# Optimization experiments

Hardware: AMD Instinct MI355X
Metric: run time of the kernel (lower is better)

## Reference

```python
import jax, jax.numpy as jnp
import numpy as np

IN_FEATURE = 256
OUT_FEATURE = 128
ALPHA = 0.5  # LeakyReLU negative slope
NEG_BIG = -9e15


def setup_inputs() -> dict:
    key = jax.random.key(0)
    k1, k2, k3, k4 = jax.random.split(key, 4)
    N = 8192
    x = jax.random.normal(k1, (N, IN_FEATURE), dtype=jnp.float32)
    adj = jax.random.randint(k2, (N, N), 0, 2, dtype=jnp.int32)
    stdv = 1.0 / np.sqrt(OUT_FEATURE)
    W = jax.random.uniform(k3, (IN_FEATURE, OUT_FEATURE), dtype=jnp.float32,
                           minval=-stdv, maxval=stdv)
    a = jax.random.uniform(k4, (2 * OUT_FEATURE, 1), dtype=jnp.float32,
                           minval=-stdv, maxval=stdv)
    return {"input": x, "adj": adj, "W": W, "a": a}


def reference(input, adj, W, a):
    # h: [N, F_out]
    h = input @ W
    # Additive attention: cat([h_i, h_j]) @ a == h_i @ a1 + h_j @ a2
    a1 = a[:OUT_FEATURE, 0]   # [F_out]
    a2 = a[OUT_FEATURE:, 0]   # [F_out]
    f1 = h @ a1               # [N]  (row / source contribution)
    f2 = h @ a2               # [N]  (col / target contribution)
    e = jax.nn.leaky_relu(f1[:, None] + f2[None, :], negative_slope=ALPHA)  # [N, N]
    scores = jnp.where(adj > 0, e, NEG_BIG)
    attention = jax.nn.softmax(scores, axis=1)  # [N, N]
    h_prime = attention @ h                     # [N, F_out]
    return jax.nn.elu(h_prime)
```

## Files before the change

### kernel.cpp

```cpp
#include <hip/hip_runtime.h>

#define N_NODES 8192
#define IN_F 256
#define OUT_F 128
#define ALPHA 0.5f
#define JC 8
#define KCHUNK 1024
#define ROUNDS 32

using short8 = __attribute__((ext_vector_type(8))) short;
using f32x4  = __attribute__((ext_vector_type(4))) float;

__device__ __forceinline__ unsigned int f2bf(float f){
  unsigned int u = __float_as_uint(f);
  u += 0x7fffu + ((u >> 16) & 1u);
  return u >> 16;
}

__global__ __launch_bounds__(256) void k_hfp(const float* __restrict__ x,
                                             const float* __restrict__ W,
                                             const float* __restrict__ a,
                                             float* __restrict__ f1,
                                             float* __restrict__ f2,
                                             unsigned short* __restrict__ P){
  __shared__ float xs[32*IN_F];
  __shared__ unsigned short hl[32*136];
  const int tid = threadIdx.x;
  const int r0 = blockIdx.x * 32;
  const float4* xg = (const float4*)(x + (size_t)r0*IN_F);
  #pragma unroll
  for(int i=0;i<8;i++) ((float4*)xs)[tid + i*256] = xg[tid + i*256];
  __syncthreads();
  const int wave = tid >> 6, lane = tid & 63;
  float2 acc[8];
  #pragma unroll
  for(int j=0;j<8;j++){ acc[j].x = 0.f; acc[j].y = 0.f; }
  const float2* Wp = (const float2*)W;
  for(int k4=0;k4<IN_F;k4+=4){
    float4 xq[8];
    #pragma unroll
    for(int j=0;j<8;j++) xq[j] = *(const float4*)&xs[(wave*8+j)*IN_F + k4];
    #pragma unroll
    for(int kk=0;kk<4;kk++){
      float2 wv = Wp[(size_t)(k4+kk)*64 + lane];
      #pragma unroll
      for(int j=0;j<8;j++){
        float xv = kk==0?xq[j].x : kk==1?xq[j].y : kk==2?xq[j].z : xq[j].w;
        acc[j].x += xv*wv.x; acc[j].y += xv*wv.y;
      }
    }
  }
  {
    float2 a1 = ((const float2*)a)[lane];
    float2 a2 = ((const float2*)(a + OUT_F))[lane];
    float s1[8], s2[8];
    #pragma unroll
    for(int j=0;j<8;j++){
      s1[j] = acc[j].x*a1.x + acc[j].y*a1.y;
      s2[j] = acc[j].x*a2.x + acc[j].y*a2.y;
    }
    #pragma unroll
    for(int off=32; off; off>>=1){
      #pragma unroll
      for(int j=0;j<8;j++){
        s1[j] += __shfl_down(s1[j], off);
        s2[j] += __shfl_down(s2[j], off);
      }
    }
    if(lane == 0){
      #pragma unroll
      for(int j=0;j<8;j++){
        f1[r0 + wave*8 + j] = s1[j];
        f2[r0 + wave*8 + j] = s2[j];
      }
    }
  }
  #pragma unroll
  for(int j=0;j<8;j++){
    unsigned int u = f2bf(acc[j].x) | (f2bf(acc[j].y) << 16);
    *(unsigned int*)&hl[(wave*8+j)*136 + 2*lane] = u;
  }
  __syncthreads();
  #pragma unroll
  for(int i=0;i<2;i++){
    int o = tid*2 + i;
    int c = o >> 6, ln = o & 63;
    int q = ln >> 4, n = ln & 15;
    short8 v;
    #pragma unroll
    for(int t=0;t<8;t++) v[t] = (short)hl[(q*8+t)*136 + c*16 + n];
    *(short8*)(P + ((size_t)(blockIdx.x*8 + c)*64 + ln)*8) = v;
  }
}

__global__ __launch_bounds__(256) void k_comp(const int* __restrict__ adj,
                                              unsigned long long* __restrict__ bm){
  const int lane = threadIdx.x & 63;
  const int wid = (blockIdx.x*256 + threadIdx.x) >> 6;
  const int nw = (gridDim.x*256) >> 6;
  const size_t total = (size_t)N_NODES*N_NODES;
  for(size_t base = (size_t)wid*512; base < total; base += (size_t)nw*512){
    unsigned long long msk[8];
    #pragma unroll
    for(int u=0;u<8;u++){
      int v = adj[base + (size_t)u*64 + lane];
      msk[u] = __ballot(v > 0);
    }
    if(lane < 8){
      unsigned long long v = msk[0];
      #pragma unroll
      for(int u=1;u<8;u++) v = (lane == u) ? msk[u] : v;
      bm[base/64 + lane] = v;
    }
  }
}

__global__ __launch_bounds__(256, 2) void k_attn(
    const unsigned int* __restrict__ bmw,
    const unsigned short* __restrict__ P,
    const float* __restrict__ f1, const float* __restrict__ f2,
    float* __restrict__ part, float* __restrict__ denp){
  __shared__ unsigned int bs[128*32];
  __shared__ float f2s[KCHUNK];
  __shared__ float f1s[128];
  __shared__ __align__(16) short Bst[2][4096];
  const int tid = threadIdx.x;
  const int wave = tid >> 6, lane = tid & 63;
  const int m = lane & 15, q = lane >> 4;
  const int jc = blockIdx.x;
  const int r0b = blockIdx.y * 128;

  ((float4*)f2s)[tid] = ((const float4*)(f2 + jc*KCHUNK))[tid];
  if(tid < 128) f1s[tid] = f1[r0b + tid];
  {
    const int row = tid >> 1, h16 = (tid & 1) * 16;
    const unsigned int* src = bmw + (size_t)(r0b + row)*256 + jc*32 + h16;
    const int sw = row & 31;
    #pragma unroll
    for(int i=0;i<16;i+=4){
      uint4 v = *(const uint4*)(src + i);
      bs[row*32 + ((h16+i  ) ^ sw)] = v.x;
      bs[row*32 + ((h16+i+1) ^ sw)] = v.y;
      bs[row*32 + ((h16+i+2) ^ sw)] = v.z;
      bs[row*32 + ((h16+i+3) ^ sw)] = v.w;
    }
  }

  const int rg0 = wave*32 + m;
  const unsigned int* bw0 = &bs[rg0*32];
  const unsigned int* bw1 = &bs[(rg0+16)*32];
  const int x0 = rg0 & 31, x1 = (rg0+16) & 31;
  const short8* PB = (const short8*)P + (size_t)jc*ROUNDS*512;
  const int sl0 = (2*wave)*64 + lane, sl1 = sl0 + 64;

  f32x4 acc0[8], acc1[8], accd0 = {0,0,0,0}, accd1 = {0,0,0,0};
  #pragma unroll
  for(int c=0;c<8;c++){ acc0[c] = (f32x4){0,0,0,0}; acc1[c] = (f32x4){0,0,0,0}; }
  const short8 ones = {0x3F80,0x3F80,0x3F80,0x3F80,0x3F80,0x3F80,0x3F80,0x3F80};

  short8 Bp0 = PB[sl0], Bp1 = PB[sl1];
  __syncthreads();
  const float rf1a = f1s[rg0], rf1b = f1s[rg0 + 16];

  auto wc8 = [&](unsigned int bits, float4 fa, float4 fb, float rf1) -> short8 {
    float w[8]; float t;
    #define WE(i, fv)                                      \
      t = rf1 + (fv); t = fmaxf(t, ALPHA*t);               \
      w[i] = (bits & (1u<<(i))) ? __expf(t) : 0.f;
    WE(0,fa.x) WE(1,fa.y) WE(2,fa.z) WE(3,fa.w)
    WE(4,fb.x) WE(5,fb.y) WE(6,fb.z) WE(7,fb.w)
    #undef WE
    union { short8 s; uint4 u; } r;
    #pragma unroll
    for(int i=0;i<4;i++)
      r.u[i] = __builtin_amdgcn_perm(__float_as_uint(w[2*i+1]),
                                     __float_as_uint(w[2*i]), 0x07060302);
    return r.s;
  };

  for(int rd=0; rd<ROUNDS; rd++){
    short8* Bw = (short8*)Bst[rd & 1];
    Bw[sl0] = Bp0; Bw[sl1] = Bp1;
    __syncthreads();
    if(rd+1 < ROUNDS){
      Bp0 = PB[(rd+1)*512 + sl0];
      Bp1 = PB[(rd+1)*512 + sl1];
    }
    unsigned int b0 = (bw0[rd ^ x0] >> (q*8)) & 0xffu;
    unsigned int b1 = (bw1[rd ^ x1] >> (q*8)) & 0xffu;
    float4 fva = *(const float4*)(f2s + rd*32 + q*8);
    float4 fvb = *(const float4*)(f2s + rd*32 + q*8 + 4);
    short8 af0 = wc8(b0, fva, fvb, rf1a);
    short8 af1 = wc8(b1, fva, fvb, rf1b);
    const short8* Br = (const short8*)Bst[rd & 1] + lane;
    #pragma unroll
    for(int c=0;c<8;c++){
      short8 Bf = Br[c*64];
      acc0[c] = __builtin_amdgcn_mfma_f32_16x16x32_bf16(af0, Bf, acc0[c], 0,0,0);
      acc1[c] = __builtin_amdgcn_mfma_f32_16x16x32_bf16(af1, Bf, acc1[c], 0,0,0);
    }
    accd0 = __builtin_amdgcn_mfma_f32_16x16x32_bf16(af0, ones, accd0, 0,0,0);
    accd1 = __builtin_amdgcn_mfma_f32_16x16x32_bf16(af1, ones, accd1, 0,0,0);
    __syncthreads();
  }

  const int r0w = r0b + wave*32;
  if(m == 0){
    #pragma unroll
    for(int reg=0;reg<4;reg++){
      denp[(size_t)jc*N_NODES + r0w + q*4 + reg]      = accd0[reg];
      denp[(size_t)jc*N_NODES + r0w + 16 + q*4 + reg] = accd1[reg];
    }
  }
  float* pp = part + (size_t)jc*N_NODES*OUT_F;
  #pragma unroll
  for(int c=0;c<8;c++){
    #pragma unroll
    for(int reg=0;reg<4;reg++){
      pp[(size_t)(r0w + q*4 + reg)*OUT_F      + c*16 + m] = acc0[c][reg];
      pp[(size_t)(r0w + 16 + q*4 + reg)*OUT_F + c*16 + m] = acc1[c][reg];
    }
  }
}

__global__ __launch_bounds__(256) void k_out(const float* __restrict__ part,
    const float* __restrict__ denp, float* __restrict__ out){
  const int idx = blockIdx.x*256 + threadIdx.x;
  const int r = idx >> 7;
  float v = 0.f, d = 0.f;
  #pragma unroll
  for(int p=0;p<JC;p++){
    v += part[(size_t)p*N_NODES*OUT_F + idx];
    d += denp[(size_t)p*N_NODES + r];
  }
  v /= d;
  out[idx] = v > 0.f ? v : (__expf(v) - 1.f);
}

extern "C" void kernel_launch(void* const* d_in, const int* in_sizes, int n_in,
                              void* d_out, int out_size, void* d_ws, size_t ws_size,
                              hipStream_t stream){
  const float* x   = (const float*)d_in[0];
  const int*   adj = (const int*)d_in[1];
  const float* W   = (const float*)d_in[2];
  const float* a   = (const float*)d_in[3];
  char* ws = (char*)d_ws;
  unsigned short* P   = (unsigned short*)(ws + (4u<<20));
  float* f1           = (float*)(ws + (6u<<20));
  float* f2           = (float*)(ws + (6u<<20) + (32u<<10));
  float* part         = (float*)(ws + (8u<<20));
  float* denp         = (float*)(ws + (40u<<20));
  unsigned long long* bm = (unsigned long long*)(ws + (48u<<20));
  float* out          = (float*)d_out;

  k_comp<<<2048, 256, 0, stream>>>(adj, bm);
  k_hfp<<<256, 256, 0, stream>>>(x, W, a, f1, f2, P);
  k_attn<<<dim3(JC,64), 256, 0, stream>>>((const unsigned int*)bm, P, f1, f2, part, denp);
  k_out<<<(N_NODES*OUT_F)/256, 256, 0, stream>>>(part, denp, out);
}
```

Measured before the change: 446.0 us.

## Merge prep kernels, halve attention row tile, drop loop barrier, vectorize output

The adjacency bitmask compression and the h/f1/f2 projection now run in one merged launch, with the x tile staged in two halves so it needs less shared memory. The attention kernel handles 64 rows per block instead of 128, with one 16-row MFMA group per wave and a launch bound of 4 blocks per CU. It also drops the trailing per-round barrier, relying on the double-buffered B tile to keep reads and writes apart. The output kernel reads and writes float4 values. The aim is more occupancy and latency hiding in the dominant attention kernel and fewer launches, at the cost of reloading each B tile for twice as many blocks.

```diff
diff --git a/kernel.cpp b/kernel.cpp
--- a/kernel.cpp
+++ b/kernel.cpp
@@ -7,6 +7,8 @@
 #define JC 8
 #define KCHUNK 1024
 #define ROUNDS 32
+#define HFP_BLOCKS 256
+#define COMP_BLOCKS 2048
 
 using short8 = __attribute__((ext_vector_type(8))) short;
 using f32x4  = __attribute__((ext_vector_type(4))) float;
@@ -17,36 +19,67 @@
   return u >> 16;
 }
 
-__global__ __launch_bounds__(256) void k_hfp(const float* __restrict__ x,
-                                             const float* __restrict__ W,
-                                             const float* __restrict__ a,
-                                             float* __restrict__ f1,
-                                             float* __restrict__ f2,
-                                             unsigned short* __restrict__ P){
-  __shared__ float xs[32*IN_F];
+__global__ __launch_bounds__(256) void k_prep(const float* __restrict__ x,
+                                              const float* __restrict__ W,
+                                              const float* __restrict__ a,
+                                              const int* __restrict__ adj,
+                                              float* __restrict__ f1,
+                                              float* __restrict__ f2,
+                                              unsigned short* __restrict__ P,
+                                              unsigned long long* __restrict__ bm){
+  __shared__ float xs[32*128];
   __shared__ unsigned short hl[32*136];
   const int tid = threadIdx.x;
+
+  if(blockIdx.x >= HFP_BLOCKS){
+    const int lane = tid & 63;
+    const int wid = ((blockIdx.x - HFP_BLOCKS)*256 + tid) >> 6;
+    const int nw = (COMP_BLOCKS*256) >> 6;
+    const size_t total = (size_t)N_NODES*N_NODES;
+    for(size_t base = (size_t)wid*512; base < total; base += (size_t)nw*512){
+      unsigned long long msk[8];
+      #pragma unroll
+      for(int u=0;u<8;u++){
+        int v = adj[base + (size_t)u*64 + lane];
+        msk[u] = __ballot(v > 0);
+      }
+      if(lane < 8){
+        unsigned long long v = msk[0];
+        #pragma unroll
+        for(int u=1;u<8;u++) v = (lane == u) ? msk[u] : v;
+        bm[base/64 + lane] = v;
+      }
+    }
+    return;
+  }
+
   const int r0 = blockIdx.x * 32;
-  const float4* xg = (const float4*)(x + (size_t)r0*IN_F);
-  #pragma unroll
-  for(int i=0;i<8;i++) ((float4*)xs)[tid + i*256] = xg[tid + i*256];
-  __syncthreads();
   const int wave = tid >> 6, lane = tid & 63;
   float2 acc[8];
   #pragma unroll
   for(int j=0;j<8;j++){ acc[j].x = 0.f; acc[j].y = 0.f; }
   const float2* Wp = (const float2*)W;
-  for(int k4=0;k4<IN_F;k4+=4){
-    float4 xq[8];
-    #pragma unroll
-    for(int j=0;j<8;j++) xq[j] = *(const float4*)&xs[(wave*8+j)*IN_F + k4];
-    #pragma unroll
-    for(int kk=0;kk<4;kk++){
-      float2 wv = Wp[(size_t)(k4+kk)*64 + lane];
-      #pragma unroll
-      for(int j=0;j<8;j++){
-        float xv = kk==0?xq[j].x : kk==1?xq[j].y : kk==2?xq[j].z : xq[j].w;
-        acc[j].x += xv*wv.x; acc[j].y += xv*wv.y;
+  for(int half=0; half<2; half++){
+    if(half) __syncthreads();
+    #pragma unroll
+    for(int i=0;i<4;i++){
+      int s = tid + i*256;
+      int row = s >> 5, c4 = (s & 31)*4;
+      ((float4*)xs)[s] = *(const float4*)(x + (size_t)(r0+row)*IN_F + half*128 + c4);
+    }
+    __syncthreads();
+    for(int k4=0;k4<128;k4+=4){
+      float4 xq[8];
+      #pragma unroll
+      for(int j=0;j<8;j++) xq[j] = *(const float4*)&xs[(wave*8+j)*128 + k4];
+      #pragma unroll
+      for(int kk=0;kk<4;kk++){
+        float2 wv = Wp[(size_t)(half*128 + k4 + kk)*64 + lane];
+        #pragma unroll
+        for(int j=0;j<8;j++){
+          float xv = kk==0?xq[j].x : kk==1?xq[j].y : kk==2?xq[j].z : xq[j].w;
+          acc[j].x += xv*wv.x; acc[j].y += xv*wv.y;
+        }
       }
     }
   }
@@ -93,90 +126,51 @@
   }
 }
 
-__global__ __launch_bounds__(256) void k_comp(const int* __restrict__ adj,
-                                              unsigned long long* __restrict__ bm){
-  const int lane = threadIdx.x & 63;
-  const int wid = (blockIdx.x*256 + threadIdx.x) >> 6;
-  const int nw = (gridDim.x*256) >> 6;
-  const size_t total = (size_t)N_NODES*N_NODES;
-  for(size_t base = (size_t)wid*512; base < total; base += (size_t)nw*512){
-    unsigned long long msk[8];
-    #pragma unroll
-    for(int u=0;u<8;u++){
-      int v = adj[base + (size_t)u*64 + lane];
-      msk[u] = __ballot(v > 0);
-    }
-    if(lane < 8){
-      unsigned long long v = msk[0];
-      #pragma unroll
-      for(int u=1;u<8;u++) v = (lane == u) ? msk[u] : v;
-      bm[base/64 + lane] = v;
-    }
-  }
-}
-
-__global__ __launch_bounds__(256, 2) void k_attn(
+__global__ __launch_bounds__(256, 4) void k_attn(
     const unsigned int* __restrict__ bmw,
     const unsigned short* __restrict__ P,
     const float* __restrict__ f1, const float* __restrict__ f2,
     float* __restrict__ part, float* __restrict__ denp){
-  __shared__ unsigned int bs[128*32];
+  __shared__ unsigned int bs[64*32];
   __shared__ float f2s[KCHUNK];
-  __shared__ float f1s[128];
+  __shared__ float f1s[64];
   __shared__ __align__(16) short Bst[2][4096];
   const int tid = threadIdx.x;
   const int wave = tid >> 6, lane = tid & 63;
   const int m = lane & 15, q = lane >> 4;
   const int jc = blockIdx.x;
-  const int r0b = blockIdx.y * 128;
+  const int r0b = blockIdx.y * 64;
 
   ((float4*)f2s)[tid] = ((const float4*)(f2 + jc*KCHUNK))[tid];
-  if(tid < 128) f1s[tid] = f1[r0b + tid];
+  if(tid < 64) f1s[tid] = f1[r0b + tid];
   {
-    const int row = tid >> 1, h16 = (tid & 1) * 16;
-    const unsigned int* src = bmw + (size_t)(r0b + row)*256 + jc*32 + h16;
+    const int row = tid >> 2, seg = (tid & 3) * 8;
+    const unsigned int* src = bmw + (size_t)(r0b + row)*256 + jc*32 + seg;
     const int sw = row & 31;
     #pragma unroll
-    for(int i=0;i<16;i+=4){
+    for(int i=0;i<8;i+=4){
       uint4 v = *(const uint4*)(src + i);
-      bs[row*32 + ((h16+i  ) ^ sw)] = v.x;
-      bs[row*32 + ((h16+i+1) ^ sw)] = v.y;
-      bs[row*32 + ((h16+i+2) ^ sw)] = v.z;
-      bs[row*32 + ((h16+i+3) ^ sw)] = v.w;
-    }
-  }
-
-  const int rg0 = wave*32 + m;
-  const unsigned int* bw0 = &bs[rg0*32];
-  const unsigned int* bw1 = &bs[(rg0+16)*32];
-  const int x0 = rg0 & 31, x1 = (rg0+16) & 31;
+      bs[row*32 + ((seg+i  ) ^ sw)] = v.x;
+      bs[row*32 + ((seg+i+1) ^ sw)] = v.y;
+      bs[row*32 + ((seg+i+2) ^ sw)] = v.z;
+      bs[row*32 + ((seg+i+3) ^ sw)] = v.w;
+    }
+  }
+
+  const int rg0 = wave*16 + m;
+  const int x0 = rg0 & 31;
   const short8* PB = (const short8*)P + (size_t)jc*ROUNDS*512;
   const int sl0 = (2*wave)*64 + lane, sl1 = sl0 + 64;
 
-  f32x4 acc0[8], acc1[8], accd0 = {0,0,0,0}, accd1 = {0,0,0,0};
-  #pragma unroll
-  for(int c=0;c<8;c++){ acc0[c] = (f32x4){0,0,0,0}; acc1[c] = (f32x4){0,0,0,0}; }
+  f32x4 acc[8], accd = {0,0,0,0};
+  #pragma unroll
+  for(int c=0;c<8;c++) acc[c] = (f32x4){0,0,0,0};
   const short8 ones = {0x3F80,0x3F80,0x3F80,0x3F80,0x3F80,0x3F80,0x3F80,0x3F80};
 
   short8 Bp0 = PB[sl0], Bp1 = PB[sl1];
   __syncthreads();
-  const float rf1a = f1s[rg0], rf1b = f1s[rg0 + 16];
-
-  auto wc8 = [&](unsigned int bits, float4 fa, float4 fb, float rf1) -> short8 {
-    float w[8]; float t;
-    #define WE(i, fv)                                      \
-      t = rf1 + (fv); t = fmaxf(t, ALPHA*t);               \
-      w[i] = (bits & (1u<<(i))) ? __expf(t) : 0.f;
-    WE(0,fa.x) WE(1,fa.y) WE(2,fa.z) WE(3,fa.w)
-    WE(4,fb.x) WE(5,fb.y) WE(6,fb.z) WE(7,fb.w)
-    #undef WE
-    union { short8 s; uint4 u; } r;
-    #pragma unroll
-    for(int i=0;i<4;i++)
-      r.u[i] = __builtin_amdgcn_perm(__float_as_uint(w[2*i+1]),
-                                     __float_as_uint(w[2*i]), 0x07060302);
-    return r.s;
-  };
+  const float rf1 = f1s[rg0];
+  const unsigned int* bw = &bs[rg0*32];
 
   for(int rd=0; rd<ROUNDS; rd++){
     short8* Bw = (short8*)Bst[rd & 1];
@@ -186,55 +180,66 @@
       Bp0 = PB[(rd+1)*512 + sl0];
       Bp1 = PB[(rd+1)*512 + sl1];
     }
-    unsigned int b0 = (bw0[rd ^ x0] >> (q*8)) & 0xffu;
-    unsigned int b1 = (bw1[rd ^ x1] >> (q*8)) & 0xffu;
-    float4 fva = *(const float4*)(f2s + rd*32 + q*8);
-    float4 fvb = *(const float4*)(f2s + rd*32 + q*8 + 4);
-    short8 af0 = wc8(b0, fva, fvb, rf1a);
-    short8 af1 = wc8(b1, fva, fvb, rf1b);
+    unsigned int b = (bw[rd ^ x0] >> (q*8)) & 0xffu;
+    float4 fa = *(const float4*)(f2s + rd*32 + q*8);
+    float4 fb = *(const float4*)(f2s + rd*32 + q*8 + 4);
+    short8 af;
+    {
+      float w[8]; float t;
+      #define WE(i, fv)                                    \
+        t = rf1 + (fv); t = fmaxf(t, ALPHA*t);             \
+        w[i] = (b & (1u<<(i))) ? __expf(t) : 0.f;
+      WE(0,fa.x) WE(1,fa.y) WE(2,fa.z) WE(3,fa.w)
+      WE(4,fb.x) WE(5,fb.y) WE(6,fb.z) WE(7,fb.w)
+      #undef WE
+      union { short8 s; uint4 u; } r;
+      #pragma unroll
+      for(int i=0;i<4;i++)
+        r.u[i] = __builtin_amdgcn_perm(__float_as_uint(w[2*i+1]),
+                                       __float_as_uint(w[2*i]), 0x07060302);
+      af = r.s;
+    }
     const short8* Br = (const short8*)Bst[rd & 1] + lane;
     #pragma unroll
-    for(int c=0;c<8;c++){
-      short8 Bf = Br[c*64];
-      acc0[c] = __builtin_amdgcn_mfma_f32_16x16x32_bf16(af0, Bf, acc0[c], 0,0,0);
-      acc1[c] = __builtin_amdgcn_mfma_f32_16x16x32_bf16(af1, Bf, acc1[c], 0,0,0);
-    }
-    accd0 = __builtin_amdgcn_mfma_f32_16x16x32_bf16(af0, ones, accd0, 0,0,0);
-    accd1 = __builtin_amdgcn_mfma_f32_16x16x32_bf16(af1, ones, accd1, 0,0,0);
-    __syncthreads();
-  }
-
-  const int r0w = r0b + wave*32;
+    for(int c=0;c<8;c++)
+      acc[c] = __builtin_amdgcn_mfma_f32_16x16x32_bf16(af, Br[c*64], acc[c], 0,0,0);
+    accd = __builtin_amdgcn_mfma_f32_16x16x32_bf16(af, ones, accd, 0,0,0);
+  }
+
+  const int r0w = r0b + wave*16;
   if(m == 0){
     #pragma unroll
-    for(int reg=0;reg<4;reg++){
-      denp[(size_t)jc*N_NODES + r0w + q*4 + reg]      = accd0[reg];
-      denp[(size_t)jc*N_NODES + r0w + 16 + q*4 + reg] = accd1[reg];
-    }
+    for(int reg=0;reg<4;reg++)
+      denp[(size_t)jc*N_NODES + r0w + q*4 + reg] = accd[reg];
   }
   float* pp = part + (size_t)jc*N_NODES*OUT_F;
   #pragma unroll
   for(int c=0;c<8;c++){
     #pragma unroll
-    for(int reg=0;reg<4;reg++){
-      pp[(size_t)(r0w + q*4 + reg)*OUT_F      + c*16 + m] = acc0[c][reg];
-      pp[(size_t)(r0w + 16 + q*4 + reg)*OUT_F + c*16 + m] = acc1[c][reg];
-    }
+    for(int reg=0;reg<4;reg++)
+      pp[(size_t)(r0w + q*4 + reg)*OUT_F + c*16 + m] = acc[c][reg];
   }
 }
 
 __global__ __launch_bounds__(256) void k_out(const float* __restrict__ part,
     const float* __restrict__ denp, float* __restrict__ out){
-  const int idx = blockIdx.x*256 + threadIdx.x;
-  const int r = idx >> 7;
-  float v = 0.f, d = 0.f;
+  const int i4 = blockIdx.x*256 + threadIdx.x;
+  const int r = i4 >> 5;
+  float4 v = {0,0,0,0};
+  float d = 0.f;
   #pragma unroll
   for(int p=0;p<JC;p++){
-    v += part[(size_t)p*N_NODES*OUT_F + idx];
+    float4 t = ((const float4*)(part + (size_t)p*N_NODES*OUT_F))[i4];
+    v.x += t.x; v.y += t.y; v.z += t.z; v.w += t.w;
     d += denp[(size_t)p*N_NODES + r];
   }
-  v /= d;
-  out[idx] = v > 0.f ? v : (__expf(v) - 1.f);
+  float inv = 1.f / d;
+  v.x *= inv; v.y *= inv; v.z *= inv; v.w *= inv;
+  v.x = v.x > 0.f ? v.x : (__expf(v.x) - 1.f);
+  v.y = v.y > 0.f ? v.y : (__expf(v.y) - 1.f);
+  v.z = v.z > 0.f ? v.z : (__expf(v.z) - 1.f);
+  v.w = v.w > 0.f ? v.w : (__expf(v.w) - 1.f);
+  ((float4*)out)[i4] = v;
 }
 
 extern "C" void kernel_launch(void* const* d_in, const int* in_sizes, int n_in,
@@ -253,8 +258,7 @@
   unsigned long long* bm = (unsigned long long*)(ws + (48u<<20));
   float* out          = (float*)d_out;
 
-  k_comp<<<2048, 256, 0, stream>>>(adj, bm);
-  k_hfp<<<256, 256, 0, stream>>>(x, W, a, f1, f2, P);
-  k_attn<<<dim3(JC,64), 256, 0, stream>>>((const unsigned int*)bm, P, f1, f2, part, denp);
-  k_out<<<(N_NODES*OUT_F)/256, 256, 0, stream>>>(part, denp, out);
-}
+  k_prep<<<HFP_BLOCKS + COMP_BLOCKS, 256, 0, stream>>>(x, W, a, adj, f1, f2, P, bm);
+  k_attn<<<dim3(JC,128), 256, 0, stream>>>((const unsigned int*)bm, P, f1, f2, part, denp);
+  k_out<<<(N_NODES*OUT_F/4)/256, 256, 0, stream>>>(part, denp, out);
+}
```

Measured after the change: 414.0 us. 1.08x faster.

## Fuse prep kernels, drop redundant attention barrier, vectorize output reduction

Applied to the files above, without the earlier changes.

Merges the adjacency bitmask compression and the h/f1/f2 projection into a single launch, with block ranges split by role, so the two independent stages can overlap and one launch is saved. The projection now stages x through shared memory in two halves, halving its shared-memory footprint. The trailing per-round `__syncthreads` in the attention loop is removed; the double-buffered LDS tile plus the barrier after each write still keep the buffers safe, which saves one barrier per round. The final reduction kernel now handles four outputs per thread with float4 loads and stores and multiplies by a reciprocal instead of dividing.

```diff
diff --git a/kernel.cpp b/kernel.cpp
--- a/kernel.cpp
+++ b/kernel.cpp
@@ -7,6 +7,8 @@
 #define JC 8
 #define KCHUNK 1024
 #define ROUNDS 32
+#define HFP_BLOCKS 256
+#define COMP_BLOCKS 2048
 
 using short8 = __attribute__((ext_vector_type(8))) short;
 using f32x4  = __attribute__((ext_vector_type(4))) float;
@@ -17,36 +19,67 @@
   return u >> 16;
 }
 
-__global__ __launch_bounds__(256) void k_hfp(const float* __restrict__ x,
-                                             const float* __restrict__ W,
-                                             const float* __restrict__ a,
-                                             float* __restrict__ f1,
-                                             float* __restrict__ f2,
-                                             unsigned short* __restrict__ P){
-  __shared__ float xs[32*IN_F];
+__global__ __launch_bounds__(256) void k_prep(const float* __restrict__ x,
+                                              const float* __restrict__ W,
+                                              const float* __restrict__ a,
+                                              const int* __restrict__ adj,
+                                              float* __restrict__ f1,
+                                              float* __restrict__ f2,
+                                              unsigned short* __restrict__ P,
+                                              unsigned long long* __restrict__ bm){
+  __shared__ float xs[32*128];
   __shared__ unsigned short hl[32*136];
   const int tid = threadIdx.x;
+
+  if(blockIdx.x >= HFP_BLOCKS){
+    const int lane = tid & 63;
+    const int wid = ((blockIdx.x - HFP_BLOCKS)*256 + tid) >> 6;
+    const int nw = (COMP_BLOCKS*256) >> 6;
+    const size_t total = (size_t)N_NODES*N_NODES;
+    for(size_t base = (size_t)wid*512; base < total; base += (size_t)nw*512){
+      unsigned long long msk[8];
+      #pragma unroll
+      for(int u=0;u<8;u++){
+        int v = adj[base + (size_t)u*64 + lane];
+        msk[u] = __ballot(v > 0);
+      }
+      if(lane < 8){
+        unsigned long long v = msk[0];
+        #pragma unroll
+        for(int u=1;u<8;u++) v = (lane == u) ? msk[u] : v;
+        bm[base/64 + lane] = v;
+      }
+    }
+    return;
+  }
+
   const int r0 = blockIdx.x * 32;
-  const float4* xg = (const float4*)(x + (size_t)r0*IN_F);
-  #pragma unroll
-  for(int i=0;i<8;i++) ((float4*)xs)[tid + i*256] = xg[tid + i*256];
-  __syncthreads();
   const int wave = tid >> 6, lane = tid & 63;
   float2 acc[8];
   #pragma unroll
   for(int j=0;j<8;j++){ acc[j].x = 0.f; acc[j].y = 0.f; }
   const float2* Wp = (const float2*)W;
-  for(int k4=0;k4<IN_F;k4+=4){
-    float4 xq[8];
-    #pragma unroll
-    for(int j=0;j<8;j++) xq[j] = *(const float4*)&xs[(wave*8+j)*IN_F + k4];
-    #pragma unroll
-    for(int kk=0;kk<4;kk++){
-      float2 wv = Wp[(size_t)(k4+kk)*64 + lane];
-      #pragma unroll
-      for(int j=0;j<8;j++){
-        float xv = kk==0?xq[j].x : kk==1?xq[j].y : kk==2?xq[j].z : xq[j].w;
-        acc[j].x += xv*wv.x; acc[j].y += xv*wv.y;
+  for(int half=0; half<2; half++){
+    if(half) __syncthreads();
+    #pragma unroll
+    for(int i=0;i<4;i++){
+      int s = tid + i*256;
+      int row = s >> 5, c4 = (s & 31)*4;
+      ((float4*)xs)[s] = *(const float4*)(x + (size_t)(r0+row)*IN_F + half*128 + c4);
+    }
+    __syncthreads();
+    for(int k4=0;k4<128;k4+=4){
+      float4 xq[8];
+      #pragma unroll
+      for(int j=0;j<8;j++) xq[j] = *(const float4*)&xs[(wave*8+j)*128 + k4];
+      #pragma unroll
+      for(int kk=0;kk<4;kk++){
+        float2 wv = Wp[(size_t)(half*128 + k4 + kk)*64 + lane];
+        #pragma unroll
+        for(int j=0;j<8;j++){
+          float xv = kk==0?xq[j].x : kk==1?xq[j].y : kk==2?xq[j].z : xq[j].w;
+          acc[j].x += xv*wv.x; acc[j].y += xv*wv.y;
+        }
       }
     }
   }
@@ -90,28 +123,6 @@
     #pragma unroll
     for(int t=0;t<8;t++) v[t] = (short)hl[(q*8+t)*136 + c*16 + n];
     *(short8*)(P + ((size_t)(blockIdx.x*8 + c)*64 + ln)*8) = v;
-  }
-}
-
-__global__ __launch_bounds__(256) void k_comp(const int* __restrict__ adj,
-                                              unsigned long long* __restrict__ bm){
-  const int lane = threadIdx.x & 63;
-  const int wid = (blockIdx.x*256 + threadIdx.x) >> 6;
-  const int nw = (gridDim.x*256) >> 6;
-  const size_t total = (size_t)N_NODES*N_NODES;
-  for(size_t base = (size_t)wid*512; base < total; base += (size_t)nw*512){
-    unsigned long long msk[8];
-    #pragma unroll
-    for(int u=0;u<8;u++){
-      int v = adj[base + (size_t)u*64 + lane];
-      msk[u] = __ballot(v > 0);
-    }
-    if(lane < 8){
-      unsigned long long v = msk[0];
-      #pragma unroll
-      for(int u=1;u<8;u++) v = (lane == u) ? msk[u] : v;
-      bm[base/64 + lane] = v;
-    }
   }
 }
 
@@ -147,8 +158,6 @@
   }
 
   const int rg0 = wave*32 + m;
-  const unsigned int* bw0 = &bs[rg0*32];
-  const unsigned int* bw1 = &bs[(rg0+16)*32];
   const int x0 = rg0 & 31, x1 = (rg0+16) & 31;
   const short8* PB = (const short8*)P + (size_t)jc*ROUNDS*512;
   const int sl0 = (2*wave)*64 + lane, sl1 = sl0 + 64;
@@ -161,6 +170,8 @@
   short8 Bp0 = PB[sl0], Bp1 = PB[sl1];
   __syncthreads();
   const float rf1a = f1s[rg0], rf1b = f1s[rg0 + 16];
+  const unsigned int* bw0 = &bs[rg0*32];
+  const unsigned int* bw1 = &bs[(rg0+16)*32];
 
   auto wc8 = [&](unsigned int bits, float4 fa, float4 fb, float rf1) -> short8 {
     float w[8]; float t;
@@ -188,10 +199,10 @@
     }
     unsigned int b0 = (bw0[rd ^ x0] >> (q*8)) & 0xffu;
     unsigned int b1 = (bw1[rd ^ x1] >> (q*8)) & 0xffu;
-    float4 fva = *(const float4*)(f2s + rd*32 + q*8);
-    float4 fvb = *(const float4*)(f2s + rd*32 + q*8 + 4);
-    short8 af0 = wc8(b0, fva, fvb, rf1a);
-    short8 af1 = wc8(b1, fva, fvb, rf1b);
+    float4 fa = *(const float4*)(f2s + rd*32 + q*8);
+    float4 fb = *(const float4*)(f2s + rd*32 + q*8 + 4);
+    short8 af0 = wc8(b0, fa, fb, rf1a);
+    short8 af1 = wc8(b1, fa, fb, rf1b);
     const short8* Br = (const short8*)Bst[rd & 1] + lane;
     #pragma unroll
     for(int c=0;c<8;c++){
@@ -201,7 +212,6 @@
     }
     accd0 = __builtin_amdgcn_mfma_f32_16x16x32_bf16(af0, ones, accd0, 0,0,0);
     accd1 = __builtin_amdgcn_mfma_f32_16x16x32_bf16(af1, ones, accd1, 0,0,0);
-    __syncthreads();
   }
 
   const int r0w = r0b + wave*32;
@@ -225,16 +235,23 @@
 
 __global__ __launch_bounds__(256) void k_out(const float* __restrict__ part,
     const float* __restrict__ denp, float* __restrict__ out){
-  const int idx = blockIdx.x*256 + threadIdx.x;
-  const int r = idx >> 7;
-  float v = 0.f, d = 0.f;
+  const int i4 = blockIdx.x*256 + threadIdx.x;
+  const int r = i4 >> 5;
+  float4 v = {0,0,0,0};
+  float d = 0.f;
   #pragma unroll
   for(int p=0;p<JC;p++){
-    v += part[(size_t)p*N_NODES*OUT_F + idx];
+    float4 t = ((const float4*)(part + (size_t)p*N_NODES*OUT_F))[i4];
+    v.x += t.x; v.y += t.y; v.z += t.z; v.w += t.w;
     d += denp[(size_t)p*N_NODES + r];
   }
-  v /= d;
-  out[idx] = v > 0.f ? v : (__expf(v) - 1.f);
+  float inv = 1.f / d;
+  v.x *= inv; v.y *= inv; v.z *= inv; v.w *= inv;
+  v.x = v.x > 0.f ? v.x : (__expf(v.x) - 1.f);
+  v.y = v.y > 0.f ? v.y : (__expf(v.y) - 1.f);
+  v.z = v.z > 0.f ? v.z : (__expf(v.z) - 1.f);
+  v.w = v.w > 0.f ? v.w : (__expf(v.w) - 1.f);
+  ((float4*)out)[i4] = v;
 }
 
 extern "C" void kernel_launch(void* const* d_in, const int* in_sizes, int n_in,
@@ -253,8 +270,7 @@
   unsigned long long* bm = (unsigned long long*)(ws + (48u<<20));
   float* out          = (float*)d_out;
 
-  k_comp<<<2048, 256, 0, stream>>>(adj, bm);
-  k_hfp<<<256, 256, 0, stream>>>(x, W, a, f1, f2, P);
+  k_prep<<<HFP_BLOCKS + COMP_BLOCKS, 256, 0, stream>>>(x, W, a, adj, f1, f2, P, bm);
   k_attn<<<dim3(JC,64), 256, 0, stream>>>((const unsigned int*)bm, P, f1, f2, part, denp);
-  k_out<<<(N_NODES*OUT_F)/256, 256, 0, stream>>>(part, denp, out);
-}
+  k_out<<<(N_NODES*OUT_F/4)/256, 256, 0, stream>>>(part, denp, out);
+}
```

Result: faster. 412.2 us (-7.6%).
